# Kernel tuning notes

Hardware: AMD Instinct MI355X
Metric: run time of the kernel (lower is better)

The kernel has to match this reference:

```python
import jax, jax.numpy as jnp
import numpy as np

B, T, C, HS = 4, 4096, 1024, 64


def setup_inputs() -> dict:
    key = jax.random.key(0)
    kx, kq, kk, kv = jax.random.split(key, 4)
    x = jax.random.normal(kx, (B, T, C), dtype=jnp.float32)
    s = 1.0 / np.sqrt(C)
    Wq = jax.random.normal(kq, (C, HS), dtype=jnp.float32) * s
    Wk = jax.random.normal(kk, (C, HS), dtype=jnp.float32) * s
    Wv = jax.random.normal(kv, (C, HS), dtype=jnp.float32) * s
    return {"x": x, "Wq": Wq, "Wk": Wk, "Wv": Wv}


def reference(x, Wq, Wk, Wv):
    # q,k,v: [B, T, HS]
    q = x @ Wq
    k = x @ Wk
    v = x @ Wv
    scale = k.shape[-1] ** -0.5
    # full T x T causal attention scores, as the torch module materializes
    scores = jnp.einsum('bqh,bkh->bqk', q, k) * scale  # [B, T, T]
    t = x.shape[1]
    causal = jnp.tril(jnp.ones((t, t), dtype=bool))
    scores = jnp.where(causal[None, :, :], scores, -jnp.inf)
    wei = jax.nn.softmax(scores, axis=-1)  # dropout = 0.0 (eval)
    out = jnp.einsum('bqk,bkh->bqh', wei, v)  # [B, T, HS]
    return out
```

## Files before the change

### kernel.cpp

```cpp
#include <hip/hip_runtime.h>
#include <math.h>

#define BB 4
#define TT 4096
#define CC 1024
#define HS 64
#define MM (BB*TT)
#define KSPLIT 8

typedef __attribute__((ext_vector_type(8))) short short8;
typedef __attribute__((ext_vector_type(4))) float f32x4;
typedef __attribute__((ext_vector_type(4))) unsigned short ushort4v;

__device__ __forceinline__ unsigned short f2bf(float f) {
    union { float f; unsigned u; } v; v.f = f;
    return (unsigned short)((v.u + 0x7fffu + ((v.u >> 16) & 1u)) >> 16);
}

__device__ __forceinline__ unsigned cvt_pk_bf16(float lo, float hi) {
    unsigned r;
    asm("v_cvt_pk_bf16_f32 %0, %1, %2" : "=v"(r) : "v"(lo), "v"(hi));
    return r;
}

typedef __attribute__((address_space(3))) unsigned short lds_us;
typedef __attribute__((address_space(1))) const unsigned short glb_us;
__device__ __forceinline__ void g2lds16(const unsigned short* g, unsigned short* l) {
    __builtin_amdgcn_global_load_lds((glb_us*)g, (lds_us*)l, 16, 0, 0);
}

__global__ __launch_bounds__(256) void prep_kernel(
    const float* __restrict__ Wq, const float* __restrict__ Wk,
    const float* __restrict__ Wv, unsigned short* __restrict__ Wt)
{
    const int which = blockIdx.x >> 4;
    const int k0 = (blockIdx.x & 15) * 64;
    const float* __restrict__ W = (which == 0) ? Wq : (which == 1) ? Wk : Wv;
    const float scale = (which == 0) ? 0.125f : 1.0f;
    __shared__ unsigned short lds[64][65];
    const int t = threadIdx.x;
    #pragma unroll
    for (int i = 0; i < 16; i++) {
        int idx = t + 256 * i;
        int r = idx >> 6, n = idx & 63;
        lds[r][n] = f2bf(W[(size_t)(k0 + r) * 64 + n] * scale);
    }
    __syncthreads();
    #pragma unroll
    for (int i = 0; i < 16; i++) {
        int idx = t + 256 * i;
        int n = idx >> 6, r = idx & 63;
        int nrow = which * 64 + n;
        int kg = k0 + r;
        int ck = kg >> 7, kloc = kg & 127;
        Wt[(size_t)ck * 24576 + (((nrow << 7) + kloc) ^ ((nrow & 7) << 3))] = lds[r][n];
    }
}

__global__ __launch_bounds__(256, 2) void qkv_mfma(
    const float* __restrict__ x, const unsigned short* __restrict__ Wt,
    unsigned short* __restrict__ qb, unsigned short* __restrict__ kbt,
    unsigned short* __restrict__ vTt)
{
    const int rt = blockIdx.x;
    __shared__ __align__(16) unsigned short xs[32][136];
    __shared__ __align__(16) unsigned short wsf[192 * 128];

    const int t = threadIdx.x;
    const int w = t >> 6;
    const int lane = t & 63;
    const int quad = lane >> 4;
    const int c = lane & 15;

    const int c2x32 = ((c >> 2) & 1) << 5;
    const int quad2 = quad ^ (c & 3);

    float4 xreg[4];
    #pragma unroll
    for (int i = 0; i < 4; i++) {
        int idx = t + 256 * i;
        int r = idx >> 5, c4 = (idx & 31) * 4;
        xreg[i] = *(const float4*)(x + (size_t)(rt * 32 + r) * CC + c4);
    }

    f32x4 acc[2][3];
    #pragma unroll
    for (int mt = 0; mt < 2; mt++)
        #pragma unroll
        for (int j = 0; j < 3; j++) acc[mt][j] = (f32x4){0.f, 0.f, 0.f, 0.f};

    for (int ck = 0; ck < 8; ++ck) {
        __syncthreads();
        {
            const unsigned short* wgp = Wt + (size_t)ck * 24576 + t * 8;
            #pragma unroll
            for (int i = 0; i < 12; i++)
                g2lds16(wgp + i * 2048, wsf + (i * 256 + w * 64) * 8);
        }
        #pragma unroll
        for (int i = 0; i < 4; i++) {
            int idx = t + 256 * i;
            int r = idx >> 5, c4 = (idx & 31) * 4;
            ushort4v p = { f2bf(xreg[i].x), f2bf(xreg[i].y), f2bf(xreg[i].z), f2bf(xreg[i].w) };
            *(ushort4v*)&xs[r][c4] = p;
        }
        __syncthreads();

        if (ck + 1 < 8) {
            #pragma unroll
            for (int i = 0; i < 4; i++) {
                int idx = t + 256 * i;
                int r = idx >> 5, c4 = (idx & 31) * 4;
                xreg[i] = *(const float4*)(x + (size_t)(rt * 32 + r) * CC + (ck + 1) * 128 + c4);
            }
        }

        #pragma unroll
        for (int ks = 0; ks < 4; ks++) {
            short8 af[2], bf[3];
            #pragma unroll
            for (int mt = 0; mt < 2; mt++)
                af[mt] = *(const short8*)&xs[16 * mt + c][ks * 32 + quad * 8];
            #pragma unroll
            for (int j = 0; j < 3; j++)
                bf[j] = *(const short8*)&wsf[(16 * (w + 4 * j) + c) * 128 +
                                             ((ks * 32) ^ c2x32) + quad2 * 8];
            #pragma unroll
            for (int mt = 0; mt < 2; mt++)
                #pragma unroll
                for (int j = 0; j < 3; j++)
                    acc[mt][j] = __builtin_amdgcn_mfma_f32_16x16x32_bf16(af[mt], bf[j], acc[mt][j], 0, 0, 0);
        }
    }

    __syncthreads();
    const int b  = rt >> 7;
    unsigned short (*vtb)[72] = (unsigned short (*)[72])wsf;
    #pragma unroll
    for (int mt = 0; mt < 2; mt++) {
        int grow = rt * 32 + 16 * mt + quad * 4;
        #pragma unroll
        for (int reg = 0; reg < 4; reg++) {
            int trow = grow + reg;
            qb[(size_t)trow * HS + 16 * w + c] = f2bf(acc[mt][0][reg]);
            int tin = trow & 4095;
            int kt = tin >> 6, kl = tin & 63;
            int dcol = 16 * w + c;
            kbt[(size_t)(b * 64 + kt) * 4096 + kl * 64 + (dcol ^ ((kl & 7) << 3))]
                = f2bf(acc[mt][1][reg]);
            vtb[16 * w + c][16 * mt + quad * 4 + reg] = f2bf(acc[mt][2][reg]);
        }
    }
    __syncthreads();
    {
        const int t0 = (rt & 127) * 32;
        const int kt = t0 >> 6, half = (t0 >> 5) & 1;
        int d = t >> 2, c8 = (t & 3) * 8;
        short8 v0 = *(const short8*)&vtb[d][c8];
        *(short8*)(vTt + (size_t)(b * 64 + kt) * 4096 + d * 64 +
                   (((half * 32 + c8) ^ ((d & 7) << 3)))) = v0;
    }
}

__global__ __launch_bounds__(256, 3) void attn_mfma(
    const unsigned short* __restrict__ qb, const unsigned short* __restrict__ kbt,
    const unsigned short* __restrict__ vTt, float* __restrict__ Opart,
    float* __restrict__ lpart)
{
    const int bid = blockIdx.x;
    const int p   = bid >> 5;
    const int qt  = (p >= 8 && p < 16) ? (p + 8) : (31 - p);
    const int rem = bid & 31;
    const int j   = rem >> 2;
    const int b   = rem & 3;

    __shared__ __align__(16) unsigned short kv[2][2][4096];
    __shared__ unsigned short ps[4][32][72];

    const int t = threadIdx.x;
    const int w = t >> 6;
    const int lane = t & 63;
    const int quad = lane >> 4;
    const int c = lane & 15;
    const int qrow = qt * 128 + 32 * w;

    const int csw0 = (quad * 8) ^ ((c & 7) << 3);
    const int csw1 = (32 + quad * 8) ^ ((c & 7) << 3);

    short8 aq[2][2];
    #pragma unroll
    for (int mt = 0; mt < 2; mt++)
        #pragma unroll
        for (int kstep = 0; kstep < 2; kstep++)
            aq[mt][kstep] = *(const short8*)(qb + (size_t)(b * TT + qrow + 16 * mt + c) * HS + kstep * 32 + quad * 8);

    const int lastkt = 2 * qt + 1;
    const int nkt = (lastkt >= j) ? ((lastkt - j) / KSPLIT) + 1 : 0;
    const unsigned short* Ktiles = kbt + (size_t)b * 64 * 4096;
    const unsigned short* Vtiles = vTt + (size_t)b * 64 * 4096;

#define STAGE(BUF, KT) do { \
    size_t o_ = (size_t)(KT) * 4096 + t * 8; \
    g2lds16(Ktiles + o_,        &kv[BUF][0][w * 512]); \
    g2lds16(Ktiles + o_ + 2048, &kv[BUF][0][2048 + w * 512]); \
    g2lds16(Vtiles + o_,        &kv[BUF][1][w * 512]); \
    g2lds16(Vtiles + o_ + 2048, &kv[BUF][1][2048 + w * 512]); } while (0)

    float l[2][4] = {{0.f,0.f,0.f,0.f},{0.f,0.f,0.f,0.f}};
    f32x4 oacc[2][4];
    #pragma unroll
    for (int mt = 0; mt < 2; mt++)
        #pragma unroll
        for (int dt = 0; dt < 4; dt++) oacc[mt][dt] = (f32x4){0.f, 0.f, 0.f, 0.f};

#define SCORE_ST(CB, MASKC) do { \
    _Pragma("unroll") \
    for (int st = 0; st < 4; st++) { \
        f32x4 s[2]; \
        s[0] = (f32x4){0.f,0.f,0.f,0.f}; s[1] = (f32x4){0.f,0.f,0.f,0.f}; \
        { \
            short8 bf0 = *(const short8*)&kv[CB][0][(16 * st + c) * 64 + csw0]; \
            short8 bf1 = *(const short8*)&kv[CB][0][(16 * st + c) * 64 + csw1]; \
            __builtin_amdgcn_s_setprio(1); \
            s[0] = __builtin_amdgcn_mfma_f32_16x16x32_bf16(aq[0][0], bf0, s[0], 0, 0, 0); \
            s[1] = __builtin_amdgcn_mfma_f32_16x16x32_bf16(aq[1][0], bf0, s[1], 0, 0, 0); \
            s[0] = __builtin_amdgcn_mfma_f32_16x16x32_bf16(aq[0][1], bf1, s[0], 0, 0, 0); \
            s[1] = __builtin_amdgcn_mfma_f32_16x16x32_bf16(aq[1][1], bf1, s[1], 0, 0, 0); \
            __builtin_amdgcn_s_setprio(0); \
        } \
        _Pragma("unroll") \
        for (int mt = 0; mt < 2; mt++) { \
            _Pragma("unroll") \
            for (int reg = 0; reg < 4; reg++) { \
                int kg = kt0 + 16 * st + c; (void)kg; \
                int qg = qrow + 16 * mt + quad * 4 + reg; (void)qg; \
                float p_ = (MASKC) ? __expf(s[mt][reg]) : 0.f; \
                s[mt][reg] = p_; \
                l[mt][reg] += p_; \
            } \
            unsigned p01 = cvt_pk_bf16(s[mt][0], s[mt][1]); \
            unsigned p23 = cvt_pk_bf16(s[mt][2], s[mt][3]); \
            ps[w][16 * mt + quad * 4 + 0][16 * st + c] = (unsigned short)p01; \
            ps[w][16 * mt + quad * 4 + 1][16 * st + c] = (unsigned short)(p01 >> 16); \
            ps[w][16 * mt + quad * 4 + 2][16 * st + c] = (unsigned short)p23; \
            ps[w][16 * mt + quad * 4 + 3][16 * st + c] = (unsigned short)(p23 >> 16); \
        } \
    } } while (0)

    if (nkt > 0) STAGE(0, j);
    __syncthreads();

    for (int i = 0; i < nkt; i++) {
        const int cb = i & 1;
        const int kt = j + KSPLIT * i;
        const int kt0 = kt * 64;

        if (i + 1 < nkt) STAGE(cb ^ 1, kt + KSPLIT);

        if (kt0 <= qrow + 31) {
            if (kt >= 2 * qt) {
                SCORE_ST(cb, kg <= qg);
            } else {
                SCORE_ST(cb, 1);
            }

            __builtin_amdgcn_s_setprio(1);
            #pragma unroll
            for (int kstep = 0; kstep < 2; kstep++) {
                const int csw = kstep ? csw1 : csw0;
                short8 ap[2];
                #pragma unroll
                for (int mt = 0; mt < 2; mt++)
                    ap[mt] = *(const short8*)&ps[w][16 * mt + c][kstep * 32 + quad * 8];
                #pragma unroll
                for (int dt = 0; dt < 4; dt++) {
                    short8 bv = *(const short8*)&kv[cb][1][(16 * dt + c) * 64 + csw];
                    oacc[0][dt] = __builtin_amdgcn_mfma_f32_16x16x32_bf16(ap[0], bv, oacc[0][dt], 0, 0, 0);
                    oacc[1][dt] = __builtin_amdgcn_mfma_f32_16x16x32_bf16(ap[1], bv, oacc[1][dt], 0, 0, 0);
                }
            }
            __builtin_amdgcn_s_setprio(0);
        }

        __syncthreads();
    }
#undef SCORE_ST
#undef STAGE

    #pragma unroll
    for (int mt = 0; mt < 2; mt++)
        #pragma unroll
        for (int reg = 0; reg < 4; reg++)
            #pragma unroll
            for (int msk = 1; msk < 16; msk <<= 1)
                l[mt][reg] += __shfl_xor(l[mt][reg], msk);

    float* __restrict__ Oj = Opart + (size_t)j * MM * HS;
    #pragma unroll
    for (int mt = 0; mt < 2; mt++)
        #pragma unroll
        for (int dt = 0; dt < 4; dt++)
            #pragma unroll
            for (int reg = 0; reg < 4; reg++)
                Oj[(size_t)(b * TT + qrow + 16 * mt + quad * 4 + reg) * HS + 16 * dt + c] = oacc[mt][dt][reg];
    if (c == 0)
        #pragma unroll
        for (int mt = 0; mt < 2; mt++)
            #pragma unroll
            for (int reg = 0; reg < 4; reg++)
                lpart[(size_t)j * MM + b * TT + qrow + 16 * mt + quad * 4 + reg] = l[mt][reg];
}

__global__ __launch_bounds__(256) void combine_kernel(
    const float* __restrict__ Opart, const float* __restrict__ lpart,
    float* __restrict__ out)
{
    const int id = blockIdx.x * 256 + threadIdx.x;
    const int row = id >> 4;
    float l = 0.f;
    #pragma unroll
    for (int j = 0; j < KSPLIT; j++) l += lpart[(size_t)j * MM + row];
    const float4* O = (const float4*)Opart;
    const size_t stride = (size_t)MM * HS / 4;
    float4 r = {0.f, 0.f, 0.f, 0.f};
    #pragma unroll
    for (int j = 0; j < KSPLIT; j++) {
        float4 a = O[id + (size_t)j * stride];
        r.x += a.x; r.y += a.y; r.z += a.z; r.w += a.w;
    }
    float inv = 1.f / l;
    r.x *= inv; r.y *= inv; r.z *= inv; r.w *= inv;
    ((float4*)out)[id] = r;
}

extern "C" void kernel_launch(void* const* d_in, const int* in_sizes, int n_in,
                              void* d_out, int out_size, void* d_ws, size_t ws_size,
                              hipStream_t stream) {
    const float* x  = (const float*)d_in[0];
    const float* Wq = (const float*)d_in[1];
    const float* Wk = (const float*)d_in[2];
    const float* Wv = (const float*)d_in[3];
    float* out = (float*)d_out;

    unsigned short* Wt   = (unsigned short*)d_ws;
    unsigned short* qbuf = Wt + 3 * 64 * 1024;
    unsigned short* kbt  = qbuf + (size_t)MM * HS;
    unsigned short* vTt  = kbt + (size_t)MM * HS;
    float* Opart = (float*)(vTt + (size_t)MM * HS);
    float* lpart = Opart + (size_t)KSPLIT * MM * HS;

    prep_kernel<<<48, 256, 0, stream>>>(Wq, Wk, Wv, Wt);
    qkv_mfma<<<MM / 32, 256, 0, stream>>>(x, Wt, qbuf, kbt, vTt);
    attn_mfma<<<BB * (TT / 128) * KSPLIT, 256, 0, stream>>>(qbuf, kbt, vTt, Opart, lpart);
    combine_kernel<<<1024, 256, 0, stream>>>(Opart, lpart, out);
}
```

Before: 133.9 us.

## Fuse split-K combine into attention kernel via last-block atomic counter

Removes the separate combine kernel launch. Each attention block increments a per-(query tile, batch) atomic counter after writing its partial output, and the last of the KSPLIT blocks reduces the partials and writes the normalized output. Counters are zeroed in the prep kernel. This saves a launch and lets reductions overlap with other attention blocks, at the cost of threadfences, an atomic per block, and serialized tail work in the final block.

```diff
diff --git a/kernel.cpp b/kernel.cpp
--- a/kernel.cpp
+++ b/kernel.cpp
@@ -31,7 +31,8 @@
 
 __global__ __launch_bounds__(256) void prep_kernel(
     const float* __restrict__ Wq, const float* __restrict__ Wk,
-    const float* __restrict__ Wv, unsigned short* __restrict__ Wt)
+    const float* __restrict__ Wv, unsigned short* __restrict__ Wt,
+    unsigned int* __restrict__ cnt)
 {
     const int which = blockIdx.x >> 4;
     const int k0 = (blockIdx.x & 15) * 64;
@@ -39,6 +40,7 @@
     const float scale = (which == 0) ? 0.125f : 1.0f;
     __shared__ unsigned short lds[64][65];
     const int t = threadIdx.x;
+    if (blockIdx.x == 0 && t < 128) cnt[t] = 0u;
     #pragma unroll
     for (int i = 0; i < 16; i++) {
         int idx = t + 256 * i;
@@ -165,7 +167,8 @@
 __global__ __launch_bounds__(256, 3) void attn_mfma(
     const unsigned short* __restrict__ qb, const unsigned short* __restrict__ kbt,
     const unsigned short* __restrict__ vTt, float* __restrict__ Opart,
-    float* __restrict__ lpart)
+    float* __restrict__ lpart, float* __restrict__ out,
+    unsigned int* __restrict__ cnt)
 {
     const int bid = blockIdx.x;
     const int p   = bid >> 5;
@@ -176,6 +179,7 @@
 
     __shared__ __align__(16) unsigned short kv[2][2][4096];
     __shared__ unsigned short ps[4][32][72];
+    __shared__ int isLast;
 
     const int t = threadIdx.x;
     const int w = t >> 6;
@@ -309,28 +313,38 @@
             #pragma unroll
             for (int reg = 0; reg < 4; reg++)
                 lpart[(size_t)j * MM + b * TT + qrow + 16 * mt + quad * 4 + reg] = l[mt][reg];
-}
-
-__global__ __launch_bounds__(256) void combine_kernel(
-    const float* __restrict__ Opart, const float* __restrict__ lpart,
-    float* __restrict__ out)
-{
-    const int id = blockIdx.x * 256 + threadIdx.x;
-    const int row = id >> 4;
-    float l = 0.f;
-    #pragma unroll
-    for (int j = 0; j < KSPLIT; j++) l += lpart[(size_t)j * MM + row];
-    const float4* O = (const float4*)Opart;
-    const size_t stride = (size_t)MM * HS / 4;
-    float4 r = {0.f, 0.f, 0.f, 0.f};
-    #pragma unroll
-    for (int j = 0; j < KSPLIT; j++) {
-        float4 a = O[id + (size_t)j * stride];
-        r.x += a.x; r.y += a.y; r.z += a.z; r.w += a.w;
-    }
-    float inv = 1.f / l;
-    r.x *= inv; r.y *= inv; r.z *= inv; r.w *= inv;
-    ((float4*)out)[id] = r;
+
+    __threadfence();
+    if (t == 0) {
+        unsigned int old = atomicAdd(&cnt[qt * 4 + b], 1u);
+        isLast = (old == KSPLIT - 1);
+    }
+    __syncthreads();
+    if (isLast) {
+        __threadfence();
+        const int rl = t >> 1;
+        const int half = t & 1;
+        const size_t row = (size_t)b * TT + qt * 128 + rl;
+        float lsum = 0.f;
+        #pragma unroll
+        for (int jj = 0; jj < KSPLIT; jj++) lsum += lpart[(size_t)jj * MM + row];
+        const float inv = 1.f / lsum;
+        const float4* Ob = (const float4*)Opart;
+        float4* outv = (float4*)out;
+        const size_t stride4 = (size_t)MM * HS / 4;
+        const size_t rbase = row * (HS / 4) + half * 8;
+        #pragma unroll
+        for (int k = 0; k < 8; k++) {
+            float4 r = {0.f, 0.f, 0.f, 0.f};
+            #pragma unroll
+            for (int jj = 0; jj < KSPLIT; jj++) {
+                float4 a = Ob[(size_t)jj * stride4 + rbase + k];
+                r.x += a.x; r.y += a.y; r.z += a.z; r.w += a.w;
+            }
+            r.x *= inv; r.y *= inv; r.z *= inv; r.w *= inv;
+            outv[rbase + k] = r;
+        }
+    }
 }
 
 extern "C" void kernel_launch(void* const* d_in, const int* in_sizes, int n_in,
@@ -348,9 +362,9 @@
     unsigned short* vTt  = kbt + (size_t)MM * HS;
     float* Opart = (float*)(vTt + (size_t)MM * HS);
     float* lpart = Opart + (size_t)KSPLIT * MM * HS;
-
-    prep_kernel<<<48, 256, 0, stream>>>(Wq, Wk, Wv, Wt);
+    unsigned int* cnt = (unsigned int*)(lpart + (size_t)KSPLIT * MM);
+
+    prep_kernel<<<48, 256, 0, stream>>>(Wq, Wk, Wv, Wt, cnt);
     qkv_mfma<<<MM / 32, 256, 0, stream>>>(x, Wt, qbuf, kbt, vTt);
-    attn_mfma<<<BB * (TT / 128) * KSPLIT, 256, 0, stream>>>(qbuf, kbt, vTt, Opart, lpart);
-    combine_kernel<<<1024, 256, 0, stream>>>(Opart, lpart, out);
-}
+    attn_mfma<<<BB * (TT / 128) * KSPLIT, 256, 0, stream>>>(qbuf, kbt, vTt, Opart, lpart, out, cnt);
+}
```

Result: slower. 321.5 us (+140.2%).
